# Optimization experiments

Measured on AMD Instinct MI355X. Metric: run time of the kernel, lower is better.

The kernel has to match this reference:

```python
import jax, jax.numpy as jnp
import numpy as np

DIM = 1024
N_HEADS = 16
HEAD_DIM = DIM // N_HEADS
MLP_RATIO = 4
LN_EPS = 1e-5


def _layer_norm(x, w):
    xf = x.astype(jnp.float32)
    mu = jnp.mean(xf, axis=-1, keepdims=True)
    var = jnp.var(xf, axis=-1, keepdims=True)
    y = (xf - mu) / jnp.sqrt(var + LN_EPS)
    return y * w[None, None, :]


def _apply_rope(x, cos, sin):
    # x: (b, s, h, d); cos, sin: (s, d/2)
    c = jnp.concatenate([cos, cos], axis=-1)[None, :, None, :]  # (1,s,1,d)
    s_ = jnp.concatenate([sin, sin], axis=-1)[None, :, None, :]
    x1, x2 = jnp.split(x, 2, axis=-1)
    rot = jnp.concatenate([-x2, x1], axis=-1)
    return x * c + rot * s_


def setup_inputs() -> dict:
    key = jax.random.key(0)
    ks = jax.random.split(key, 12)
    b, s = 2, 2048
    x = jax.random.normal(ks[0], (b, s, DIM), dtype=jnp.float32)
    rot_cos = jax.random.uniform(ks[1], (1, s, 1, 1, HEAD_DIM), dtype=jnp.float32)
    rot_sin = jax.random.uniform(ks[2], (1, s, 1, 1, HEAD_DIM), dtype=jnp.float32)
    w_init = 0.02
    params = {
        'ln1_w': jnp.ones((DIM,), jnp.float32),
        'w_qkv': jax.random.normal(ks[3], (3 * DIM, DIM), jnp.float32) * w_init,
        'w_out': jax.random.normal(ks[4], (DIM, DIM), jnp.float32) * w_init,
        'ln2_w': jnp.ones((DIM,), jnp.float32),
        'w_mlp1': jax.random.normal(ks[5], (MLP_RATIO * DIM, DIM), jnp.float32) * w_init,
        'b_mlp1': jnp.zeros((MLP_RATIO * DIM,), jnp.float32),
        'w_mlp2': jax.random.normal(ks[6], (DIM, MLP_RATIO * DIM), jnp.float32) * w_init,
        'b_mlp2': jnp.zeros((DIM,), jnp.float32),
    }
    return {'x': x, 'rot_cos': rot_cos, 'rot_sin': rot_sin, **params}


def reference(x, rot_cos, rot_sin, ln1_w, w_qkv, w_out, ln2_w, w_mlp1, b_mlp1, w_mlp2, b_mlp2):
    b, s, _ = x.shape
    # _split_rotary: (1,s,1,1,hd) -> (s, hd/2)
    cos = rot_cos[0, :, 0, 0, : HEAD_DIM // 2]
    sin = rot_sin[0, :, 0, 0, : HEAD_DIM // 2]

    x_skip = x
    h1 = _layer_norm(x, ln1_w)
    qkv = jnp.einsum('bsd,ed->bse', h1, w_qkv).reshape(b, s, 3, N_HEADS, HEAD_DIM)
    q, k, v = qkv[:, :, 0], qkv[:, :, 1], qkv[:, :, 2]
    q = _apply_rope(q, cos, sin)
    k = _apply_rope(k, cos, sin)

    # causal SDPA, scale = 1/sqrt(head_dim) (flex_attention default)
    scale = 1.0 / np.sqrt(HEAD_DIM)
    scores = jnp.einsum('bqhd,bkhd->bhqk', q, k) * scale
    causal = jnp.tril(jnp.ones((s, s), dtype=bool))
    scores = jnp.where(causal[None, None], scores, -jnp.inf)
    attn = jax.nn.softmax(scores, axis=-1)
    o = jnp.einsum('bhqk,bkhd->bqhd', attn, v).reshape(b, s, DIM)

    # attn out + residual (eval: dropout off, scale=1)
    x = x_skip + jnp.einsum('bsd,ed->bse', o, w_out)

    # MLP with tanh GELU + residual
    h2 = _layer_norm(x, ln2_w)
    u = jnp.einsum('bsd,ed->bse', h2, w_mlp1) + b_mlp1
    u = jax.nn.gelu(u, approximate=True)
    m = jnp.einsum('bse,de->bsd', u, w_mlp2) + b_mlp2
    return x + m
```

## Files before the change

### kernel.cpp

```cpp
#include <hip/hip_runtime.h>
#include <hip/hip_bf16.h>
#include <math.h>


#define B_ 2
#define S_ 2048
#define D_ 1024
#define H_ 16
#define DH_ 64
#define MLP_ 4096
#define ROWS_ (B_ * S_)

typedef short bf16x8 __attribute__((ext_vector_type(8)));
typedef float f32x4 __attribute__((ext_vector_type(4)));
typedef unsigned short ushort_t;
typedef ushort_t u16x4 __attribute__((ext_vector_type(4)));
typedef unsigned int u32x2 __attribute__((ext_vector_type(2)));

__device__ __forceinline__ float wave_reduce_sum(float v) {
  #pragma unroll
  for (int off = 32; off > 0; off >>= 1) v += __shfl_down(v, off, 64);
  return v;
}

__device__ __forceinline__ ushort_t f2bf(float v) {
  __hip_bfloat16 h = __float2bfloat16(v);
  return *(ushort_t*)&h;
}
__device__ __forceinline__ float bf2f(ushort_t u) {
  unsigned int v = ((unsigned int)u) << 16;
  union { unsigned int i; float f; } c; c.i = v; return c.f;
}

__device__ __forceinline__ float exp2_fast(float x) {
#if __has_builtin(__builtin_amdgcn_exp2f)
  return __builtin_amdgcn_exp2f(x);
#else
  return exp2f(x);
#endif
}

__device__ __forceinline__ void async_copy16(const void* g, void* l) {
  __builtin_amdgcn_global_load_lds(
      (const __attribute__((address_space(1))) void*)g,
      (__attribute__((address_space(3))) void*)l, 16, 0, 0);
}

__global__ __launch_bounds__(256) void cast_w_kernel(
    const float* __restrict__ s0, ushort_t* __restrict__ d0, int n0,
    const float* __restrict__ s1, ushort_t* __restrict__ d1, int n1,
    const float* __restrict__ s2, ushort_t* __restrict__ d2, int n2,
    const float* __restrict__ s3, ushort_t* __restrict__ d3, int n3) {
  const float* s; ushort_t* d; int n;
  switch (blockIdx.y) {
    case 0: s = s0; d = d0; n = n0; break;
    case 1: s = s1; d = d1; n = n1; break;
    case 2: s = s2; d = d2; n = n2; break;
    default: s = s3; d = d3; n = n3; break;
  }
  const int i = (blockIdx.x * 256 + threadIdx.x) * 4;
  if (i < n) {
    const float4 v = *reinterpret_cast<const float4*>(s + i);
    u16x4 o;
    o[0] = f2bf(v.x); o[1] = f2bf(v.y); o[2] = f2bf(v.z); o[3] = f2bf(v.w);
    *reinterpret_cast<u16x4*>(d + i) = o;
  }
}

__global__ __launch_bounds__(256) void ln_kernel(
    const float* __restrict__ x, const float* __restrict__ w,
    ushort_t* __restrict__ y) {
  const int row = blockIdx.x;
  const float4 v = reinterpret_cast<const float4*>(x + (size_t)row * D_)[threadIdx.x];
  float s  = v.x + v.y + v.z + v.w;
  float ss = v.x * v.x + v.y * v.y + v.z * v.z + v.w * v.w;
  __shared__ float red[8];
  const int wave = threadIdx.x >> 6, lane = threadIdx.x & 63;
  const float ws1 = wave_reduce_sum(s);
  const float ws2 = wave_reduce_sum(ss);
  if (lane == 0) { red[wave] = ws1; red[4 + wave] = ws2; }
  __syncthreads();
  const float tot  = red[0] + red[1] + red[2] + red[3];
  const float tot2 = red[4] + red[5] + red[6] + red[7];
  const float mu  = tot * (1.0f / D_);
  const float var = tot2 * (1.0f / D_) - mu * mu;
  const float inv = rsqrtf(var + 1e-5f);
  const float4 wv = reinterpret_cast<const float4*>(w)[threadIdx.x];
  u16x4 o;
  o[0] = f2bf((v.x - mu) * inv * wv.x);
  o[1] = f2bf((v.y - mu) * inv * wv.y);
  o[2] = f2bf((v.z - mu) * inv * wv.z);
  o[3] = f2bf((v.w - mu) * inv * wv.w);
  reinterpret_cast<u16x4*>(y + (size_t)row * D_)[threadIdx.x] = o;
}

__device__ __forceinline__ float gelu_tanh(float u) {
  const float u3 = u * u * u;
  const float t = tanhf(0.7978845608028654f * (u + 0.044715f * u3));
  return 0.5f * u * (1.0f + t);
}

template <int FUSE, int OUTBF, int QKV>
__global__ __launch_bounds__(256) void gemm_bt(
    const ushort_t* __restrict__ A, const ushort_t* __restrict__ W,
    const float* __restrict__ bias, const float* __restrict__ res,
    void* __restrict__ Cv, ushort_t* __restrict__ VtOut,
    int M, int N, int K, int sm, int sn, int rects_n) {
  __shared__ ushort_t As[2][128 * 32];
  __shared__ ushort_t Bs[2][128 * 32];
  const int tid = threadIdx.x;
  const int wave = tid >> 6, lane = tid & 63;
  const int l15 = lane & 15, quad = lane >> 4;

  const int lin = blockIdx.x;
  const int xcd = lin & 7, j = lin >> 3;
  const int rm = xcd / rects_n, rn = xcd % rects_n;
  const int m0 = (rm * sm + (j % sm)) * 128;
  const int n0 = (rn * sn + (j / sm)) * 128;
  const int wm = (wave & 1) * 64, wn = (wave >> 1) * 64;

  const int srow = tid >> 2;
  const int gcol = (((tid & 3) ^ ((srow >> 1) & 3)) * 8);
  const ushort_t* Ag = A + (size_t)(m0 + srow) * K + gcol;
  const ushort_t* Wg = W + (size_t)(n0 + srow) * K + gcol;

  f32x4 acc[4][4] = {};
  const int rslot = (quad ^ ((l15 >> 1) & 3)) * 8;

  const int NI = K >> 5;
  async_copy16(Ag,          &As[0][tid * 8]);
  async_copy16(Ag + 64 * K, &As[0][2048 + tid * 8]);
  async_copy16(Wg,          &Bs[0][tid * 8]);
  async_copy16(Wg + 64 * K, &Bs[0][2048 + tid * 8]);

  for (int i = 0; i < NI; ++i) {
    const int st = i & 1;
    __syncthreads();
    if (i + 1 < NI) {
      const int k1 = (i + 1) << 5;
      async_copy16(Ag + k1,          &As[1 - st][tid * 8]);
      async_copy16(Ag + 64 * K + k1, &As[1 - st][2048 + tid * 8]);
      async_copy16(Wg + k1,          &Bs[1 - st][tid * 8]);
      async_copy16(Wg + 64 * K + k1, &Bs[1 - st][2048 + tid * 8]);
    }
    bf16x8 af[4], bfr[4];
    #pragma unroll
    for (int ii = 0; ii < 4; ++ii) {
      af[ii]  = *(const bf16x8*)&As[st][(wm + ii * 16 + l15) * 32 + rslot];
      bfr[ii] = *(const bf16x8*)&Bs[st][(wn + ii * 16 + l15) * 32 + rslot];
    }
    #pragma unroll
    for (int ii = 0; ii < 4; ++ii)
      #pragma unroll
      for (int jj = 0; jj < 4; ++jj)
        acc[ii][jj] = __builtin_amdgcn_mfma_f32_16x16x32_bf16(af[ii], bfr[jj], acc[ii][jj], 0, 0, 0);
  }

  #pragma unroll
  for (int i = 0; i < 4; ++i) {
    const int mb = m0 + wm + i * 16 + quad * 4;
    #pragma unroll
    for (int jj = 0; jj < 4; ++jj) {
      const int n = n0 + wn + jj * 16 + l15;
      float cv[4];
      #pragma unroll
      for (int r = 0; r < 4; ++r) {
        float c = acc[i][jj][r];
        if (FUSE & 1) c += bias[n];
        if (FUSE & 2) c = gelu_tanh(c);
        if (FUSE & 4) c += res[(size_t)(mb + r) * N + n];
        cv[r] = c;
      }
      if (QKV && ((n0 + wn) >> 10) == 2) {
        const int d  = n & 63;
        const int hh = (n >> 6) & 15;
        const int bb = mb >> 11;
        const int ss = mb & (S_ - 1);
        u16x4 pk;
        #pragma unroll
        for (int r = 0; r < 4; ++r) pk[r] = f2bf(cv[r]);
        *(u16x4*)&VtOut[((size_t)(bb * H_ + hh) * DH_ + d) * S_ + ss] = pk;
      } else {
        #pragma unroll
        for (int r = 0; r < 4; ++r) {
          if (OUTBF) ((ushort_t*)Cv)[(size_t)(mb + r) * N + n] = f2bf(cv[r]);
          else       ((float*)Cv)[(size_t)(mb + r) * N + n]   = cv[r];
        }
      }
    }
  }
}

template <int FUSE, int OUTBF>
__global__ __launch_bounds__(256) void gemm64_bt(
    const ushort_t* __restrict__ A, const ushort_t* __restrict__ W,
    const float* __restrict__ bias, const float* __restrict__ res,
    void* __restrict__ Cv, int M, int N, int K, int sm, int sn, int rects_n) {
  __shared__ ushort_t As[2][64 * 64];
  __shared__ ushort_t Bs[2][128 * 64];
  const int tid = threadIdx.x;
  const int wave = tid >> 6, lane = tid & 63;
  const int l15 = lane & 15, quad = lane >> 4;

  const int lin = blockIdx.x;
  const int xcd = lin & 7, j = lin >> 3;
  const int rm = xcd / rects_n, rn = xcd % rects_n;
  const int m0 = (rm * sm + (j % sm)) * 64;
  const int n0 = (rn * sn + (j / sm)) * 128;
  const int wn = wave * 32;

  const int srow = tid >> 3;
  const int gcol = (((tid & 7) ^ (srow & 7)) * 8);
  const ushort_t* Ag = A + (size_t)(m0 + srow) * K + gcol;
  const ushort_t* Wg = W + (size_t)(n0 + srow) * K + gcol;

  f32x4 acc[4][2] = {};

  const int NI = K >> 6;
  #pragma unroll
  for (int i = 0; i < 2; ++i)
    async_copy16(Ag + (size_t)i * 32 * K, &As[0][i * 2048 + tid * 8]);
  #pragma unroll
  for (int i = 0; i < 4; ++i)
    async_copy16(Wg + (size_t)i * 32 * K, &Bs[0][i * 2048 + tid * 8]);

  for (int it = 0; it < NI; ++it) {
    const int st = it & 1;
    __syncthreads();
    if (it + 1 < NI) {
      const int k1 = (it + 1) << 6;
      #pragma unroll
      for (int i = 0; i < 2; ++i)
        async_copy16(Ag + (size_t)i * 32 * K + k1, &As[1 - st][i * 2048 + tid * 8]);
      #pragma unroll
      for (int i = 0; i < 4; ++i)
        async_copy16(Wg + (size_t)i * 32 * K + k1, &Bs[1 - st][i * 2048 + tid * 8]);
    }
    #pragma unroll
    for (int kk = 0; kk < 2; ++kk) {
      const int slot = (((kk * 4 + quad) ^ (l15 & 7)) * 8);
      bf16x8 af[4], bfr[2];
      #pragma unroll
      for (int i = 0; i < 4; ++i)
        af[i] = *(const bf16x8*)&As[st][(i * 16 + l15) * 64 + slot];
      #pragma unroll
      for (int jj = 0; jj < 2; ++jj)
        bfr[jj] = *(const bf16x8*)&Bs[st][(wn + jj * 16 + l15) * 64 + slot];
      #pragma unroll
      for (int i = 0; i < 4; ++i)
        #pragma unroll
        for (int jj = 0; jj < 2; ++jj)
          acc[i][jj] = __builtin_amdgcn_mfma_f32_16x16x32_bf16(af[i], bfr[jj], acc[i][jj], 0, 0, 0);
    }
  }

  #pragma unroll
  for (int i = 0; i < 4; ++i) {
    const int mb = m0 + i * 16 + quad * 4;
    #pragma unroll
    for (int jj = 0; jj < 2; ++jj) {
      const int n = n0 + wn + jj * 16 + l15;
      #pragma unroll
      for (int r = 0; r < 4; ++r) {
        float c = acc[i][jj][r];
        if (FUSE & 1) c += bias[n];
        if (FUSE & 2) c = gelu_tanh(c);
        if (FUSE & 4) c += res[(size_t)(mb + r) * N + n];
        if (OUTBF) ((ushort_t*)Cv)[(size_t)(mb + r) * N + n] = f2bf(c);
        else       ((float*)Cv)[(size_t)(mb + r) * N + n]   = c;
      }
    }
  }
}

__global__ __launch_bounds__(256) void rope_kernel(
    const ushort_t* __restrict__ qkv, const float* __restrict__ cosb,
    const float* __restrict__ sinb, ushort_t* __restrict__ Qo,
    ushort_t* __restrict__ Ko) {
  const int bs = blockIdx.x;
  const int s  = bs & (S_ - 1);
  const int b  = bs >> 11;
  const int t  = threadIdx.x;
  const ushort_t* base = qkv + (size_t)bs * (3 * D_);
  #pragma unroll
  for (int i = 0; i < 8; ++i) {
    const int e = i * 256 + t;
    const int which = e >> 10;
    const int rem = e & 1023;
    const int h = rem >> 6;
    const int d = rem & 63;
    const float val = bf2f(base[e]);
    float out;
    if (d < 32) {
      out = val * cosb[s * 64 + d] - bf2f(base[e + 32]) * sinb[s * 64 + d];
    } else {
      out = val * cosb[s * 64 + d - 32] + bf2f(base[e - 32]) * sinb[s * 64 + d - 32];
    }
    const size_t oidx = (((size_t)(b * H_ + h)) * S_ + s) * DH_ + d;
    if (which == 0) Qo[oidx] = f2bf(out * 0.18033688736f);
    else            Ko[oidx] = f2bf(out);
  }
}

#define PPAD 72

__global__ __launch_bounds__(256) void attn_kernel(
    const ushort_t* __restrict__ Qb, const ushort_t* __restrict__ Kb,
    const ushort_t* __restrict__ Vt, ushort_t* __restrict__ O) {
  __shared__ ushort_t Ks[2][64 * 64];
  __shared__ ushort_t Vs[2][64 * 64];
  __shared__ ushort_t Plds[4][2][16 * PPAD];

  const int tid  = threadIdx.x;
  const int wave = tid >> 6;
  const int lane = tid & 63;
  const int l15 = lane & 15, quad = lane >> 4;

  const int lin = blockIdx.x;
  const int bh  = lin & 31;
  const int g   = 15 - (lin >> 5);
  const int b = bh >> 4, h = bh & 15;
  const int q0 = g * 128 + wave * 32;

  const int nch_w   = (q0 >> 6) + 1;
  const int nch_max = 2 * g + 2;

  const ushort_t* Kbh = Kb + (size_t)bh * S_ * DH_;
  const ushort_t* Vbh = Vt + (size_t)bh * DH_ * S_;

  auto stage = [&](int buf, int c) {
    const int k0s = c << 6;
    #pragma unroll
    for (int i = 0; i < 2; ++i) {
      const int idx  = i * 256 + tid;
      const int row  = idx >> 3;
      const int slot = idx & 7;
      const int scol = ((slot ^ (row & 7)) * 8);
      async_copy16(Kbh + (size_t)(k0s + row) * DH_ + scol, &Ks[buf][idx * 8]);
      async_copy16(Vbh + (size_t)row * S_ + k0s + scol,    &Vs[buf][idx * 8]);
    }
  };

  bf16x8 qb[2][2];
  #pragma unroll
  for (int t = 0; t < 2; ++t) {
    const ushort_t* qptr = Qb + ((size_t)bh * S_ + q0 + t * 16 + l15) * DH_ + quad * 8;
    qb[t][0] = *(const bf16x8*)(qptr);
    qb[t][1] = *(const bf16x8*)(qptr + 32);
  }

  f32x4 o_acc[2][4] = {};
  float m_run[2] = {-1e30f, -1e30f}, l_run[2] = {0.0f, 0.0f};

  stage(0, 0);

  for (int c = 0; c < nch_max; ++c) {
    const int st = c & 1;
    __syncthreads();
    if (c + 1 < nch_max) stage(st ^ 1, c + 1);
    if (c >= nch_w) continue;
    const int k0 = c << 6;

    bf16x8 ka[4][2];
    #pragma unroll
    for (int kt = 0; kt < 4; ++kt) {
      const int row = kt * 16 + l15;
      const int bse = row * 64, rx = row & 7;
      ka[kt][0] = *(const bf16x8*)&Ks[st][bse + ((quad ^ rx) * 8)];
      ka[kt][1] = *(const bf16x8*)&Ks[st][bse + (((4 + quad) ^ rx) * 8)];
    }

    f32x4 s_t[2][4];
    __builtin_amdgcn_s_setprio(1);
    #pragma unroll
    for (int t = 0; t < 2; ++t)
      #pragma unroll
      for (int kt = 0; kt < 4; ++kt) {
        f32x4 z = {0.0f, 0.0f, 0.0f, 0.0f};
        z = __builtin_amdgcn_mfma_f32_16x16x32_bf16(ka[kt][0], qb[t][0], z, 0, 0, 0);
        z = __builtin_amdgcn_mfma_f32_16x16x32_bf16(ka[kt][1], qb[t][1], z, 0, 0, 0);
        s_t[t][kt] = z;
      }
    __builtin_amdgcn_s_setprio(0);

    if (c == nch_w - 1) {
      #pragma unroll
      for (int t = 0; t < 2; ++t) {
        const int query = q0 + t * 16 + l15;
        #pragma unroll
        for (int kt = 0; kt < 4; ++kt)
          #pragma unroll
          for (int r = 0; r < 4; ++r)
            if (k0 + kt * 16 + quad * 4 + r > query) s_t[t][kt][r] = -1e30f;
      }
    }

    #pragma unroll
    for (int t = 0; t < 2; ++t) {
      float mx = -1e30f;
      #pragma unroll
      for (int kt = 0; kt < 4; ++kt)
        #pragma unroll
        for (int r = 0; r < 4; ++r) mx = fmaxf(mx, s_t[t][kt][r]);
      mx = fmaxf(mx, __shfl_xor(mx, 16, 64));
      mx = fmaxf(mx, __shfl_xor(mx, 32, 64));
      const float m_new = fmaxf(m_run[t], mx);
      const float alpha = exp2_fast(m_run[t] - m_new);
      float rs = 0.0f;
      #pragma unroll
      for (int kt = 0; kt < 4; ++kt)
        #pragma unroll
        for (int r = 0; r < 4; ++r) {
          const float e = exp2_fast(s_t[t][kt][r] - m_new);
          s_t[t][kt][r] = e;
          rs += e;
        }
      rs += __shfl_xor(rs, 16, 64);
      rs += __shfl_xor(rs, 32, 64);
      l_run[t] = l_run[t] * alpha + rs;
      m_run[t] = m_new;
      #pragma unroll
      for (int mt = 0; mt < 4; ++mt)
        #pragma unroll
        for (int r = 0; r < 4; ++r) o_acc[t][mt][r] *= alpha;
    }

    bf16x8 va[4][2];
    #pragma unroll
    for (int mt = 0; mt < 4; ++mt) {
      const int row = mt * 16 + l15;
      const int bse = row * 64, rx = row & 7;
      va[mt][0] = *(const bf16x8*)&Vs[st][bse + ((quad ^ rx) * 8)];
      va[mt][1] = *(const bf16x8*)&Vs[st][bse + (((4 + quad) ^ rx) * 8)];
    }

    #pragma unroll
    for (int t = 0; t < 2; ++t) {
      ushort_t* Pw = &Plds[wave][t][0];
      #pragma unroll
      for (int kt = 0; kt < 4; ++kt) {
        u32x2 wpair;
        wpair[0] = (unsigned)f2bf(s_t[t][kt][0]) | ((unsigned)f2bf(s_t[t][kt][1]) << 16);
        wpair[1] = (unsigned)f2bf(s_t[t][kt][2]) | ((unsigned)f2bf(s_t[t][kt][3]) << 16);
        *(u32x2*)&Pw[l15 * PPAD + kt * 16 + quad * 4] = wpair;
      }
      asm volatile("s_waitcnt lgkmcnt(0)" ::: "memory");
      const bf16x8 pb0 = *(const bf16x8*)&Pw[l15 * PPAD + quad * 8];
      const bf16x8 pb1 = *(const bf16x8*)&Pw[l15 * PPAD + 32 + quad * 8];
      __builtin_amdgcn_s_setprio(1);
      #pragma unroll
      for (int mt = 0; mt < 4; ++mt) {
        o_acc[t][mt] = __builtin_amdgcn_mfma_f32_16x16x32_bf16(va[mt][0], pb0, o_acc[t][mt], 0, 0, 0);
        o_acc[t][mt] = __builtin_amdgcn_mfma_f32_16x16x32_bf16(va[mt][1], pb1, o_acc[t][mt], 0, 0, 0);
      }
      __builtin_amdgcn_s_setprio(0);
    }
  }

  #pragma unroll
  for (int t = 0; t < 2; ++t) {
    const float inv = 1.0f / l_run[t];
    #pragma unroll
    for (int mt = 0; mt < 4; ++mt) {
      u16x4 pk;
      #pragma unroll
      for (int r = 0; r < 4; ++r) pk[r] = f2bf(o_acc[t][mt][r] * inv);
      *(u16x4*)&O[(((size_t)b * S_ + q0 + t * 16 + l15) * H_ + h) * DH_ + mt * 16 + quad * 4] = pk;
    }
  }
}

extern "C" void kernel_launch(void* const* d_in, const int* in_sizes, int n_in,
                              void* d_out, int out_size, void* d_ws, size_t ws_size,
                              hipStream_t stream) {
  const float* x       = (const float*)d_in[0];
  const float* rot_cos = (const float*)d_in[1];
  const float* rot_sin = (const float*)d_in[2];
  const float* ln1_w   = (const float*)d_in[3];
  const float* w_qkv   = (const float*)d_in[4];
  const float* w_out   = (const float*)d_in[5];
  const float* ln2_w   = (const float*)d_in[6];
  const float* w_mlp1  = (const float*)d_in[7];
  const float* b_mlp1  = (const float*)d_in[8];
  const float* w_mlp2  = (const float*)d_in[9];
  const float* b_mlp2  = (const float*)d_in[10];
  float* out = (float*)d_out;

  char* wsb = (char*)d_ws;
  const size_t MB = 1u << 20;
  ushort_t* h1_bf  = (ushort_t*)(wsb + 0 * MB);
  ushort_t* qkv_bf = (ushort_t*)(wsb + 8 * MB);
  ushort_t* q_bf   = (ushort_t*)(wsb + 32 * MB);
  ushort_t* k_bf   = (ushort_t*)(wsb + 40 * MB);
  ushort_t* v_t    = (ushort_t*)(wsb + 48 * MB);
  ushort_t* o_bf   = (ushort_t*)(wsb + 56 * MB);
  float*    x2     = (float*)   (wsb + 64 * MB);
  ushort_t* u_bf   = (ushort_t*)(wsb + 80 * MB);
  ushort_t* wq_bf  = (ushort_t*)(wsb + 112 * MB);
  ushort_t* wo_bf  = (ushort_t*)(wsb + 118 * MB);
  ushort_t* w1_bf  = (ushort_t*)(wsb + 120 * MB);
  ushort_t* w2_bf  = (ushort_t*)(wsb + 128 * MB);
  (void)ws_size; (void)in_sizes; (void)n_in; (void)out_size;

  dim3 b256(256);

  cast_w_kernel<<<dim3(4096, 4), b256, 0, stream>>>(
      w_qkv, wq_bf, 3 * D_ * D_, w_out, wo_bf, D_ * D_,
      w_mlp1, w1_bf, MLP_ * D_, w_mlp2, w2_bf, MLP_ * D_);
  ln_kernel<<<dim3(ROWS_), b256, 0, stream>>>(x, ln1_w, h1_bf);
  gemm_bt<0, 1, 1><<<dim3(768), b256, 0, stream>>>(
      h1_bf, wq_bf, nullptr, nullptr, qkv_bf, v_t, ROWS_, 3 * D_, D_, 16, 6, 4);
  rope_kernel<<<dim3(ROWS_), b256, 0, stream>>>(qkv_bf, rot_cos, rot_sin, q_bf, k_bf);
  attn_kernel<<<dim3(512), b256, 0, stream>>>(q_bf, k_bf, v_t, o_bf);
  gemm64_bt<4, 0><<<dim3(512), b256, 0, stream>>>(
      o_bf, wo_bf, nullptr, x, x2, ROWS_, D_, D_, 16, 4, 2);
  ln_kernel<<<dim3(ROWS_), b256, 0, stream>>>(x2, ln2_w, h1_bf);
  gemm_bt<3, 1, 0><<<dim3(1024), b256, 0, stream>>>(
      h1_bf, w1_bf, b_mlp1, nullptr, u_bf, nullptr, ROWS_, MLP_, D_, 16, 8, 4);
  gemm64_bt<5, 0><<<dim3(512), b256, 0, stream>>>(
      u_bf, w2_bf, b_mlp2, x2, out, ROWS_, D_, MLP_, 16, 4, 2);
}
```

Before: 376.6 us.

## Triple-buffer GEMM LDS pipeline with explicit vmcnt waits; fast exp-based GELU

```diff
diff --git a/kernel.cpp b/kernel.cpp
--- a/kernel.cpp
+++ b/kernel.cpp
@@ -37,6 +37,13 @@
   return __builtin_amdgcn_exp2f(x);
 #else
   return exp2f(x);
+#endif
+}
+__device__ __forceinline__ float rcp_fast(float x) {
+#if __has_builtin(__builtin_amdgcn_rcpf)
+  return __builtin_amdgcn_rcpf(x);
+#else
+  return 1.0f / x;
 #endif
 }
 
@@ -95,9 +102,9 @@
 }
 
 __device__ __forceinline__ float gelu_tanh(float u) {
-  const float u3 = u * u * u;
-  const float t = tanhf(0.7978845608028654f * (u + 0.044715f * u3));
-  return 0.5f * u * (1.0f + t);
+  const float p = u + 0.044715f * u * u * u;
+  const float e = exp2_fast(-2.3022078f * p);
+  return u * rcp_fast(1.0f + e);
 }
 
 template <int FUSE, int OUTBF, int QKV>
@@ -106,8 +113,8 @@
     const float* __restrict__ bias, const float* __restrict__ res,
     void* __restrict__ Cv, ushort_t* __restrict__ VtOut,
     int M, int N, int K, int sm, int sn, int rects_n) {
-  __shared__ ushort_t As[2][128 * 32];
-  __shared__ ushort_t Bs[2][128 * 32];
+  __shared__ ushort_t As[3][128 * 32];
+  __shared__ ushort_t Bs[3][128 * 32];
   const int tid = threadIdx.x;
   const int wave = tid >> 6, lane = tid & 63;
   const int l15 = lane & 15, quad = lane >> 4;
@@ -128,20 +135,30 @@
   const int rslot = (quad ^ ((l15 >> 1) & 3)) * 8;
 
   const int NI = K >> 5;
-  async_copy16(Ag,          &As[0][tid * 8]);
-  async_copy16(Ag + 64 * K, &As[0][2048 + tid * 8]);
-  async_copy16(Wg,          &Bs[0][tid * 8]);
-  async_copy16(Wg + 64 * K, &Bs[0][2048 + tid * 8]);
-
+  async_copy16(Ag,               &As[0][tid * 8]);
+  async_copy16(Ag + 64 * K,      &As[0][2048 + tid * 8]);
+  async_copy16(Wg,               &Bs[0][tid * 8]);
+  async_copy16(Wg + 64 * K,      &Bs[0][2048 + tid * 8]);
+  if (NI > 1) {
+    async_copy16(Ag + 32,          &As[1][tid * 8]);
+    async_copy16(Ag + 64 * K + 32, &As[1][2048 + tid * 8]);
+    async_copy16(Wg + 32,          &Bs[1][tid * 8]);
+    async_copy16(Wg + 64 * K + 32, &Bs[1][2048 + tid * 8]);
+  }
+
+  int st = 0;
   for (int i = 0; i < NI; ++i) {
-    const int st = i & 1;
-    __syncthreads();
-    if (i + 1 < NI) {
-      const int k1 = (i + 1) << 5;
-      async_copy16(Ag + k1,          &As[1 - st][tid * 8]);
-      async_copy16(Ag + 64 * K + k1, &As[1 - st][2048 + tid * 8]);
-      async_copy16(Wg + k1,          &Bs[1 - st][tid * 8]);
-      async_copy16(Wg + 64 * K + k1, &Bs[1 - st][2048 + tid * 8]);
+    if (i + 1 < NI) asm volatile("s_waitcnt vmcnt(4)" ::: "memory");
+    else            asm volatile("s_waitcnt vmcnt(0)" ::: "memory");
+    __builtin_amdgcn_s_barrier();
+    __builtin_amdgcn_sched_barrier(0);
+    if (i + 2 < NI) {
+      const int k2 = (i + 2) << 5;
+      const int nb = (st >= 1) ? st - 1 : st + 2;
+      async_copy16(Ag + k2,          &As[nb][tid * 8]);
+      async_copy16(Ag + 64 * K + k2, &As[nb][2048 + tid * 8]);
+      async_copy16(Wg + k2,          &Bs[nb][tid * 8]);
+      async_copy16(Wg + 64 * K + k2, &Bs[nb][2048 + tid * 8]);
     }
     bf16x8 af[4], bfr[4];
     #pragma unroll
@@ -154,6 +171,7 @@
       #pragma unroll
       for (int jj = 0; jj < 4; ++jj)
         acc[ii][jj] = __builtin_amdgcn_mfma_f32_16x16x32_bf16(af[ii], bfr[jj], acc[ii][jj], 0, 0, 0);
+    st = (st == 2) ? 0 : st + 1;
   }
 
   #pragma unroll
```

Measured after the change: 364.4 us. -3.2%, faster.
